# Optimization experiments

Measured on AMD Instinct MI355X. Metric: run time of the kernel, lower is better.

Reference implementation:

```python
import jax, jax.numpy as jnp
import numpy as np

N_NODES = 100000
D_FEAT = 128
N_EDGES = 1500000
H1 = 2 * D_FEAT  # 256, input to first linear (concat of src/dst feats)
H2 = 128


def setup_inputs() -> dict:
    key = jax.random.key(0)
    k_x, k_e, k_w1, k_w2 = jax.random.split(key, 4)
    x = jax.random.normal(k_x, (N_NODES, D_FEAT), dtype=jnp.float32)
    edge_label_index = jax.random.randint(k_e, (2, N_EDGES), 0, N_NODES, dtype=jnp.int64)
    # Kaiming-ish small init for stability
    W1 = jax.random.normal(k_w1, (H1, H2), dtype=jnp.float32) * (1.0 / np.sqrt(H1))
    b1 = jnp.zeros((H2,), dtype=jnp.float32)
    W2 = jax.random.normal(k_w2, (H2, 1), dtype=jnp.float32) * (1.0 / np.sqrt(H2))
    b2 = jnp.zeros((1,), dtype=jnp.float32)
    return {"x": x, "edge_label_index": edge_label_index,
            "W1": W1, "b1": b1, "W2": W2, "b2": b2}


def reference(x, edge_label_index, W1, b1, W2, b2):
    row, col = edge_label_index[0], edge_label_index[1]
    # gather node pair features and concat: [E, 2*D]
    h = jnp.concatenate([x[row], x[col]], axis=-1)
    h = jax.nn.relu(h @ W1 + b1)  # [E, H2]
    out = h @ W2 + b2             # [E, 1]
    return out.reshape(-1)        # [E]
```

## Files before the change

### kernel.cpp

```cpp
#include <hip/hip_runtime.h>
#include <hip/hip_bf16.h>
#include <stdint.h>

typedef __attribute__((ext_vector_type(8))) short s16x8;
typedef __attribute__((ext_vector_type(8))) unsigned short u16x8;
typedef __attribute__((ext_vector_type(4))) float f32x4;

#define D_FEAT 128
#define H2 128

__device__ __forceinline__ unsigned short f2bf(float f) {
  uint32_t u = __float_as_uint(f);
  return (unsigned short)((u + 0x7fffu + ((u >> 16) & 1u)) >> 16);
}
__device__ __forceinline__ float bf2f(unsigned short s) {
  return __uint_as_float((uint32_t)s << 16);
}

__global__ void k_cvt_w1(const float* __restrict__ W1, unsigned short* __restrict__ w1s) {
  int tid = blockIdx.x * blockDim.x + threadIdx.x;
  int lane = tid & 63;
  int kkf  = tid >> 6;
  int kk = kkf >> 3, f = kkf & 7;
  int c = lane & 15, g = lane >> 4;
  int n = f * 16 + c;
  u16x8 o;
#pragma unroll
  for (int j = 0; j < 8; ++j)
    o[j] = f2bf(W1[(kk * 32 + g * 8 + j) * H2 + n]);
  ((u16x8*)w1s)[tid] = o;
}

__global__ void k_cvt_w2p(const float* __restrict__ W2, float* __restrict__ w2p) {
  int s = threadIdx.x;
  w2p[s] = W2[(s & 7) * 16 + (s >> 3)];
}

__global__ __launch_bounds__(256, 4)
void k_uv(const float* __restrict__ x,
          const unsigned short* __restrict__ w1ws,
          const float* __restrict__ b1,
          unsigned short* __restrict__ u,
          unsigned short* __restrict__ v,
          int nNodes)
{
  __shared__ alignas(16) unsigned short w1t[H2 * 256];
  const int t0 = threadIdx.x, lane = t0 & 63, wid = t0 >> 6;
  const int c = lane & 15, g = lane >> 4;

#pragma unroll
  for (int i = 0; i < 16; ++i) {
    int idx = i * 256 + t0;
    ((u16x8*)w1t)[idx] = ((const u16x8*)w1ws)[idx];
  }

  const int nb = blockIdx.x * 128 + wid * 32;
  s16x8 af[4][2];
#pragma unroll
  for (int m = 0; m < 2; ++m) {
    int node = nb + m * 16 + c;
    node = node < nNodes ? node : nNodes - 1;
    const float* xp = x + (size_t)node * D_FEAT;
#pragma unroll
    for (int kk = 0; kk < 4; ++kk) {
      const f32x4* q = (const f32x4*)(xp + kk * 32 + g * 8);
      f32x4 a = q[0], b = q[1];
      s16x8 vv;
      vv[0] = (short)f2bf(a[0]); vv[1] = (short)f2bf(a[1]);
      vv[2] = (short)f2bf(a[2]); vv[3] = (short)f2bf(a[3]);
      vv[4] = (short)f2bf(b[0]); vv[5] = (short)f2bf(b[1]);
      vv[6] = (short)f2bf(b[2]); vv[7] = (short)f2bf(b[3]);
      af[kk][m] = vv;
    }
  }
  float b1v[8];
#pragma unroll
  for (int f = 0; f < 8; ++f) b1v[f] = b1[f * 16 + c];

  __syncthreads();
  const unsigned short* bbase = w1t + (unsigned)lane * 8;

  f32x4 acc[2][8];

#pragma unroll
  for (int m = 0; m < 2; ++m)
#pragma unroll
    for (int f = 0; f < 8; ++f) {
      f32x4 z = {b1v[f], b1v[f], b1v[f], b1v[f]};
      acc[m][f] = z;
    }
#pragma unroll
  for (int kk = 0; kk < 4; ++kk)
#pragma unroll
    for (int f = 0; f < 8; ++f) {
      s16x8 bfrag = *(const s16x8*)(bbase + (kk * 8 + f) * 512);
#pragma unroll
      for (int m = 0; m < 2; ++m)
        acc[m][f] = __builtin_amdgcn_mfma_f32_16x16x32_bf16(af[kk][m], bfrag, acc[m][f], 0, 0, 0);
    }
#pragma unroll
  for (int m = 0; m < 2; ++m)
#pragma unroll
    for (int r = 0; r < 4; ++r) {
      int node = nb + m * 16 + g * 4 + r;
      if (node < nNodes) {
        u16x8 o;
#pragma unroll
        for (int f = 0; f < 8; ++f) o[f] = f2bf(acc[m][f][r]);
        *(u16x8*)(u + (size_t)node * H2 + c * 8) = o;
      }
    }

#pragma unroll
  for (int m = 0; m < 2; ++m)
#pragma unroll
    for (int f = 0; f < 8; ++f) {
      f32x4 z = {0.f, 0.f, 0.f, 0.f};
      acc[m][f] = z;
    }
#pragma unroll
  for (int kk = 0; kk < 4; ++kk)
#pragma unroll
    for (int f = 0; f < 8; ++f) {
      s16x8 bfrag = *(const s16x8*)(bbase + ((kk + 4) * 8 + f) * 512);
#pragma unroll
      for (int m = 0; m < 2; ++m)
        acc[m][f] = __builtin_amdgcn_mfma_f32_16x16x32_bf16(af[kk][m], bfrag, acc[m][f], 0, 0, 0);
    }
#pragma unroll
  for (int m = 0; m < 2; ++m)
#pragma unroll
    for (int r = 0; r < 4; ++r) {
      int node = nb + m * 16 + g * 4 + r;
      if (node < nNodes) {
        u16x8 o;
#pragma unroll
        for (int f = 0; f < 8; ++f) o[f] = f2bf(acc[m][f][r]);
        *(u16x8*)(v + (size_t)node * H2 + c * 8) = o;
      }
    }
}

__global__ __launch_bounds__(256, 8)
void k_edge(const unsigned short* __restrict__ u,
            const unsigned short* __restrict__ v,
            const int* __restrict__ eli,
            const float* __restrict__ w2p,
            const float* __restrict__ b2,
            float* __restrict__ out, int E, int nNodes)
{
  const int t0 = threadIdx.x, lane = t0 & 63, wid = t0 >> 6;
  const int p  = lane & 15;
  const int eo = lane >> 4;
  const int ewave = blockIdx.x * 32 + wid * 8;

  u16x8 uu[2], vv[2];
  int eidx[2];
#pragma unroll
  for (int m = 0; m < 2; ++m) {
    int e = ewave + m * 4 + eo;
    eidx[m] = e;
    int ec = e < E ? e : E - 1;
    int nr = eli[ec], nc = eli[E + ec];
    nr = nr < 0 ? 0 : (nr >= nNodes ? nNodes - 1 : nr);
    nc = nc < 0 ? 0 : (nc >= nNodes ? nNodes - 1 : nc);
    uu[m] = *(const u16x8*)(u + (size_t)nr * H2 + p * 8);
    vv[m] = *(const u16x8*)(v + (size_t)nc * H2 + p * 8);
  }

  const f32x4* wq = (const f32x4*)(w2p + p * 8);
  const f32x4 w0 = wq[0], w1 = wq[1];
  const float b2s = b2[0];

#pragma unroll
  for (int m = 0; m < 2; ++m) {
    float s = 0.f;
#pragma unroll
    for (int j = 0; j < 8; ++j) {
      float h = bf2f(uu[m][j]) + bf2f(vv[m][j]);
      h = h > 0.f ? h : 0.f;
      float w = (j < 4) ? w0[j & 3] : w1[j & 3];
      s += h * w;
    }
    s += __shfl_xor(s, 1, 64);
    s += __shfl_xor(s, 2, 64);
    s += __shfl_xor(s, 4, 64);
    s += __shfl_xor(s, 8, 64);
    if (p == 0 && eidx[m] < E) out[eidx[m]] = s + b2s;
  }
}

__global__ __launch_bounds__(512, 4)
void k_fallback(const float* __restrict__ xf,
                const int* __restrict__ eli,
                const float* __restrict__ W1,
                const float* __restrict__ b1,
                const float* __restrict__ W2,
                const float* __restrict__ b2,
                float* __restrict__ out, int E, int nNodes)
{
  __shared__ alignas(16) unsigned short w1t[H2 * 256];
  const int t0 = threadIdx.x, lane = t0 & 63, wid = t0 >> 6;
  const int c = lane & 15, g = lane >> 4;

#pragma unroll
  for (int i = 0; i < 8; ++i) {
    int chunk = i * 512 + t0;
    int cl = chunk & 63, kkf = chunk >> 6;
    int kk = kkf >> 3, f = kkf & 7;
    int cc = cl & 15, gg = cl >> 4;
    int n = f * 16 + cc;
    u16x8 o;
#pragma unroll
    for (int j = 0; j < 8; ++j)
      o[j] = f2bf(W1[(kk * 32 + gg * 8 + j) * H2 + n]);
    ((u16x8*)w1t)[chunk] = o;
  }

  const int gbase = blockIdx.x * 256 + wid * 32;
  unsigned ro[2], co[2];
#pragma unroll
  for (int m = 0; m < 2; ++m) {
    int e = gbase + m * 16 + c;
    e = e < E ? e : E - 1;
    int nr = eli[e], nc = eli[E + e];
    nr = nr < 0 ? 0 : (nr >= nNodes ? nNodes - 1 : nr);
    nc = nc < 0 ? 0 : (nc >= nNodes ? nNodes - 1 : nc);
    ro[m] = (unsigned)nr * D_FEAT + g * 8;
    co[m] = (unsigned)nc * D_FEAT + g * 8;
  }
  __syncthreads();

  auto loadA = [&](int kk, s16x8* dst) {
#pragma unroll
    for (int m = 0; m < 2; ++m) {
      unsigned off = (kk < 4 ? ro[m] : co[m]) + (unsigned)((kk & 3) * 32);
      const f32x4* q = (const f32x4*)(xf + off);
      f32x4 a = q[0], b = q[1];
      s16x8 vv2;
      vv2[0] = (short)f2bf(a[0]); vv2[1] = (short)f2bf(a[1]);
      vv2[2] = (short)f2bf(a[2]); vv2[3] = (short)f2bf(a[3]);
      vv2[4] = (short)f2bf(b[0]); vv2[5] = (short)f2bf(b[1]);
      vv2[6] = (short)f2bf(b[2]); vv2[7] = (short)f2bf(b[3]);
      dst[m] = vv2;
    }
  };

  f32x4 acc[2][8];
#pragma unroll
  for (int m = 0; m < 2; ++m)
#pragma unroll
    for (int f = 0; f < 8; ++f) {
      f32x4 z = {0.f, 0.f, 0.f, 0.f};
      acc[m][f] = z;
    }
  s16x8 abuf[2][2];
  loadA(0, abuf[0]);
  loadA(1, abuf[1]);
  const unsigned short* bbase = w1t + (unsigned)lane * 8;
#pragma unroll
  for (int kk = 0; kk < 8; ++kk) {
#pragma unroll
    for (int f = 0; f < 8; ++f) {
      s16x8 bfrag = *(const s16x8*)(bbase + (kk * 8 + f) * 512);
#pragma unroll
      for (int m = 0; m < 2; ++m)
        acc[m][f] = __builtin_amdgcn_mfma_f32_16x16x32_bf16(abuf[kk & 1][m], bfrag, acc[m][f], 0, 0, 0);
    }
    if (kk < 6) loadA(kk + 2, abuf[kk & 1]);
  }
  float b1v[8], w2v[8];
#pragma unroll
  for (int f = 0; f < 8; ++f) { b1v[f] = b1[f * 16 + c]; w2v[f] = W2[f * 16 + c]; }
  const float b2s = b2[0];
#pragma unroll
  for (int m = 0; m < 2; ++m) {
    float sr[4];
#pragma unroll
    for (int r = 0; r < 4; ++r) {
      float s = 0.f;
#pragma unroll
      for (int f = 0; f < 8; ++f) {
        float h = acc[m][f][r] + b1v[f];
        h = h > 0.f ? h : 0.f;
        s += h * w2v[f];
      }
#pragma unroll
      for (int msk = 1; msk < 16; msk <<= 1) s += __shfl_xor(s, msk, 64);
      sr[r] = s;
    }
    int ebase2 = gbase + m * 16 + g * 4;
    if (c == 0 && ebase2 < E) {
      f32x4 o = {sr[0] + b2s, sr[1] + b2s, sr[2] + b2s, sr[3] + b2s};
      *(f32x4*)(out + ebase2) = o;
    }
  }
}

extern "C" void kernel_launch(void* const* d_in, const int* in_sizes, int n_in,
                              void* d_out, int out_size, void* d_ws, size_t ws_size,
                              hipStream_t stream) {
  const float* x   = (const float*)d_in[0];
  const int*   eli = (const int*)d_in[1];
  const float* W1  = (const float*)d_in[2];
  const float* b1  = (const float*)d_in[3];
  const float* W2  = (const float*)d_in[4];
  const float* b2  = (const float*)d_in[5];
  float* out = (float*)d_out;

  const int E      = in_sizes[1] / 2;
  const int nNodes = in_sizes[0] / D_FEAT;

  const size_t ubytes = (size_t)nNodes * H2 * 2;
  const size_t need   = 2 * ubytes + 65536 + 512;

  if (ws_size >= need) {
    unsigned short* us  = (unsigned short*)d_ws;
    unsigned short* vs  = (unsigned short*)((char*)d_ws + ubytes);
    unsigned short* w1f = (unsigned short*)((char*)d_ws + 2 * ubytes);
    float*          w2p = (float*)((char*)d_ws + 2 * ubytes + 65536);

    k_cvt_w1<<<16, 256, 0, stream>>>(W1, w1f);
    k_cvt_w2p<<<1, 128, 0, stream>>>(W2, w2p);
    k_uv<<<(nNodes + 127) / 128, 256, 0, stream>>>(x, w1f, b1, us, vs, nNodes);
    k_edge<<<(E + 31) / 32, 256, 0, stream>>>(us, vs, eli, w2p, b2, out, E, nNodes);
  } else {
    k_fallback<<<(E + 255) / 256, 512, 0, stream>>>(x, eli, W1, b1, W2, b2, out, E, nNodes);
  }
}
```

Baseline: 129.9 us.

## Store node projections as fp16 and use packed dot2 with DPP reductions

Switches the intermediate per-node u/v projections from bf16 to fp16 so the edge kernel can do packed half add/relu and fdot2 accumulation against fp16 W2. The cross-lane sum moves from shuffles to DPP adds. Each wave now handles 16 edges instead of 8, and the two weight-conversion kernels are merged into one launch. The goal is less ALU work and launch overhead in the gather-bound edge kernel, at the cost of fp16 range and precision limits on the hidden activations.

```diff
diff --git a/kernel.cpp b/kernel.cpp
--- a/kernel.cpp
+++ b/kernel.cpp
@@ -5,6 +5,8 @@
 typedef __attribute__((ext_vector_type(8))) short s16x8;
 typedef __attribute__((ext_vector_type(8))) unsigned short u16x8;
 typedef __attribute__((ext_vector_type(4))) float f32x4;
+typedef __attribute__((ext_vector_type(8))) _Float16 h16x8;
+typedef __attribute__((ext_vector_type(2))) _Float16 h16x2;
 
 #define D_FEAT 128
 #define H2 128
@@ -13,35 +15,44 @@
   uint32_t u = __float_as_uint(f);
   return (unsigned short)((u + 0x7fffu + ((u >> 16) & 1u)) >> 16);
 }
-__device__ __forceinline__ float bf2f(unsigned short s) {
-  return __uint_as_float((uint32_t)s << 16);
-}
-
-__global__ void k_cvt_w1(const float* __restrict__ W1, unsigned short* __restrict__ w1s) {
-  int tid = blockIdx.x * blockDim.x + threadIdx.x;
-  int lane = tid & 63;
-  int kkf  = tid >> 6;
-  int kk = kkf >> 3, f = kkf & 7;
-  int c = lane & 15, g = lane >> 4;
-  int n = f * 16 + c;
-  u16x8 o;
-#pragma unroll
-  for (int j = 0; j < 8; ++j)
-    o[j] = f2bf(W1[(kk * 32 + g * 8 + j) * H2 + n]);
-  ((u16x8*)w1s)[tid] = o;
-}
-
-__global__ void k_cvt_w2p(const float* __restrict__ W2, float* __restrict__ w2p) {
-  int s = threadIdx.x;
-  w2p[s] = W2[(s & 7) * 16 + (s >> 3)];
+
+__device__ __forceinline__ float dot2acc(h16x2 a, h16x2 b, float c) {
+#if __has_builtin(__builtin_amdgcn_fdot2)
+  return __builtin_amdgcn_fdot2(a, b, c, false);
+#else
+  return c + (float)a.x * (float)b.x + (float)a.y * (float)b.y;
+#endif
+}
+
+#define DPP_ADD(s, ctrl) \
+  ((s) + __int_as_float(__builtin_amdgcn_update_dpp(0, __float_as_int(s), (ctrl), 0xF, 0xF, true)))
+
+__global__ void k_cvt(const float* __restrict__ W1, const float* __restrict__ W2,
+                      unsigned short* __restrict__ w1s, _Float16* __restrict__ w2h) {
+  if (blockIdx.x < 16) {
+    int tid = blockIdx.x * 256 + threadIdx.x;
+    int lane = tid & 63;
+    int kkf  = tid >> 6;
+    int kk = kkf >> 3, f = kkf & 7;
+    int c = lane & 15, g = lane >> 4;
+    int n = f * 16 + c;
+    u16x8 o;
+#pragma unroll
+    for (int j = 0; j < 8; ++j)
+      o[j] = f2bf(W1[(kk * 32 + g * 8 + j) * H2 + n]);
+    ((u16x8*)w1s)[tid] = o;
+  } else {
+    int s = threadIdx.x;
+    if (s < 128) w2h[s] = (_Float16)W2[(s & 7) * 16 + (s >> 3)];
+  }
 }
 
 __global__ __launch_bounds__(256, 4)
 void k_uv(const float* __restrict__ x,
           const unsigned short* __restrict__ w1ws,
           const float* __restrict__ b1,
-          unsigned short* __restrict__ u,
-          unsigned short* __restrict__ v,
+          _Float16* __restrict__ u,
+          _Float16* __restrict__ v,
           int nNodes)
 {
   __shared__ alignas(16) unsigned short w1t[H2 * 256];
@@ -104,10 +115,10 @@
     for (int r = 0; r < 4; ++r) {
       int node = nb + m * 16 + g * 4 + r;
       if (node < nNodes) {
-        u16x8 o;
-#pragma unroll
-        for (int f = 0; f < 8; ++f) o[f] = f2bf(acc[m][f][r]);
-        *(u16x8*)(u + (size_t)node * H2 + c * 8) = o;
+        h16x8 o;
+#pragma unroll
+        for (int f = 0; f < 8; ++f) o[f] = (_Float16)acc[m][f][r];
+        *(h16x8*)(u + (size_t)node * H2 + c * 8) = o;
       }
     }
 
@@ -133,59 +144,59 @@
     for (int r = 0; r < 4; ++r) {
       int node = nb + m * 16 + g * 4 + r;
       if (node < nNodes) {
-        u16x8 o;
-#pragma unroll
-        for (int f = 0; f < 8; ++f) o[f] = f2bf(acc[m][f][r]);
-        *(u16x8*)(v + (size_t)node * H2 + c * 8) = o;
+        h16x8 o;
+#pragma unroll
+        for (int f = 0; f < 8; ++f) o[f] = (_Float16)acc[m][f][r];
+        *(h16x8*)(v + (size_t)node * H2 + c * 8) = o;
       }
     }
 }
 
 __global__ __launch_bounds__(256, 8)
-void k_edge(const unsigned short* __restrict__ u,
-            const unsigned short* __restrict__ v,
+void k_edge(const _Float16* __restrict__ u,
+            const _Float16* __restrict__ v,
             const int* __restrict__ eli,
-            const float* __restrict__ w2p,
+            const _Float16* __restrict__ w2h,
             const float* __restrict__ b2,
             float* __restrict__ out, int E, int nNodes)
 {
   const int t0 = threadIdx.x, lane = t0 & 63, wid = t0 >> 6;
   const int p  = lane & 15;
   const int eo = lane >> 4;
-  const int ewave = blockIdx.x * 32 + wid * 8;
-
-  u16x8 uu[2], vv[2];
-  int eidx[2];
-#pragma unroll
-  for (int m = 0; m < 2; ++m) {
+  const int ewave = blockIdx.x * 64 + wid * 16;
+
+  const h16x8 wv = *(const h16x8*)(w2h + p * 8);
+  const float b2s = b2[0];
+
+  h16x8 uu[4], vv[4];
+  int eidx[4];
+#pragma unroll
+  for (int m = 0; m < 4; ++m) {
     int e = ewave + m * 4 + eo;
     eidx[m] = e;
     int ec = e < E ? e : E - 1;
     int nr = eli[ec], nc = eli[E + ec];
     nr = nr < 0 ? 0 : (nr >= nNodes ? nNodes - 1 : nr);
     nc = nc < 0 ? 0 : (nc >= nNodes ? nNodes - 1 : nc);
-    uu[m] = *(const u16x8*)(u + (size_t)nr * H2 + p * 8);
-    vv[m] = *(const u16x8*)(v + (size_t)nc * H2 + p * 8);
-  }
-
-  const f32x4* wq = (const f32x4*)(w2p + p * 8);
-  const f32x4 w0 = wq[0], w1 = wq[1];
-  const float b2s = b2[0];
-
-#pragma unroll
-  for (int m = 0; m < 2; ++m) {
+    uu[m] = *(const h16x8*)(u + (size_t)nr * H2 + p * 8);
+    vv[m] = *(const h16x8*)(v + (size_t)nc * H2 + p * 8);
+  }
+
+  const h16x8 z8 = {};
+#pragma unroll
+  for (int m = 0; m < 4; ++m) {
+    h16x8 h8 = __builtin_elementwise_max(uu[m] + vv[m], z8);
     float s = 0.f;
 #pragma unroll
-    for (int j = 0; j < 8; ++j) {
-      float h = bf2f(uu[m][j]) + bf2f(vv[m][j]);
-      h = h > 0.f ? h : 0.f;
-      float w = (j < 4) ? w0[j & 3] : w1[j & 3];
-      s += h * w;
-    }
-    s += __shfl_xor(s, 1, 64);
-    s += __shfl_xor(s, 2, 64);
-    s += __shfl_xor(s, 4, 64);
-    s += __shfl_xor(s, 8, 64);
+    for (int t = 0; t < 4; ++t) {
+      h16x2 hp = {h8[2 * t], h8[2 * t + 1]};
+      h16x2 wp = {wv[2 * t], wv[2 * t + 1]};
+      s = dot2acc(hp, wp, s);
+    }
+    s = DPP_ADD(s, 0xB1);
+    s = DPP_ADD(s, 0x4E);
+    s = DPP_ADD(s, 0x141);
+    s = DPP_ADD(s, 0x140);
     if (p == 0 && eidx[m] < E) out[eidx[m]] = s + b2s;
   }
 }
@@ -315,15 +326,14 @@
   const size_t need   = 2 * ubytes + 65536 + 512;
 
   if (ws_size >= need) {
-    unsigned short* us  = (unsigned short*)d_ws;
-    unsigned short* vs  = (unsigned short*)((char*)d_ws + ubytes);
+    _Float16*       us  = (_Float16*)d_ws;
+    _Float16*       vs  = (_Float16*)((char*)d_ws + ubytes);
     unsigned short* w1f = (unsigned short*)((char*)d_ws + 2 * ubytes);
-    float*          w2p = (float*)((char*)d_ws + 2 * ubytes + 65536);
-
-    k_cvt_w1<<<16, 256, 0, stream>>>(W1, w1f);
-    k_cvt_w2p<<<1, 128, 0, stream>>>(W2, w2p);
+    _Float16*       w2h = (_Float16*)((char*)d_ws + 2 * ubytes + 65536);
+
+    k_cvt<<<17, 256, 0, stream>>>(W1, W2, w1f, w2h);
     k_uv<<<(nNodes + 127) / 128, 256, 0, stream>>>(x, w1f, b1, us, vs, nNodes);
-    k_edge<<<(E + 31) / 32, 256, 0, stream>>>(us, vs, eli, w2p, b2, out, E, nNodes);
+    k_edge<<<(E + 63) / 64, 256, 0, stream>>>(us, vs, eli, w2h, b2, out, E, nNodes);
   } else {
     k_fallback<<<(E + 255) / 256, 512, 0, stream>>>(x, eli, W1, b1, W2, b2, out, E, nNodes);
   }
```

New measurement: 129.5 us. About the same (-0.3%).
